# Kernel tuning notes

Hardware: AMD Instinct MI355X
Metric: run time of the kernel (lower is better)

## Reference

```python
import jax, jax.numpy as jnp
import numpy as np

ALPHA, ETA, THETA = 0.999, 0.6, 0.05
EPS = 1e-12  # torch F.normalize eps

def silu(x):
    return x * jax.nn.sigmoid(x)

def l2norm(x):
    # torch.nn.functional.normalize(x) : p=2, dim=1
    n = jnp.linalg.norm(x, axis=1, keepdims=True)
    return x / jnp.maximum(n, EPS)

def mlp(params, x):
    # layers[0]: Linear(16,32)+SiLU ; layers[1]: Linear(32,16)+SiLU
    W0, b0, W1, b1 = params
    h = silu(x @ W0.T + b0)
    return silu(h @ W1.T + b1)

def setup_inputs() -> dict:
    key = jax.random.key(0)
    ks = jax.random.split(key, 8)
    N, D, H = 1048576, 16, 32
    def w(k, shape):
        fan_in = shape[1]
        return jax.random.normal(k, shape, jnp.float32) / np.float32(np.sqrt(fan_in))
    return {
        'X':  jax.random.normal(ks[0], (N, D), jnp.float32),
        'W0': w(ks[1], (H, D)),
        'b0': jnp.zeros((H,), jnp.float32),
        'W1': w(ks[2], (D, H)),
        'b1': jnp.zeros((D,), jnp.float32),
        'WK': w(ks[3], (D, D)),
        'WV': w(ks[4], (D, D)),
        'WQ': w(ks[5], (D, D)),
    }

def reference(X, W0, b0, W1, b1, WK, WV, WQ):
    # ---- update(X): test-time gradient write into the tiny MLP memory ----
    x = jax.lax.stop_gradient(X)            # X.detach()
    v = jax.lax.stop_gradient(silu(x @ WV.T))     # with torch.no_grad()
    q = l2norm(silu(x @ WQ.T))              # normalize(silu(Q(x)))

    def loss_fn(p):
        y = mlp(p, q)
        return jnp.mean((y - v) ** 2)

    g = jax.grad(loss_fn)((W0, b0, W1, b1))
    # surprise starts empty -> zeros; surprise = eta*0 - theta*g = -theta*g
    # update_params = alpha*base.detach() + surprise.detach()
    new_params = tuple(jax.lax.stop_gradient(ALPHA * p - THETA * gi)
                       for p, gi in zip((W0, b0, W1, b1), g))

    # ---- retrieve(X, new_params): key-value read ----
    # note order differs from update: silu(normalize(Q(X)))
    r_in = silu(l2norm(X @ WQ.T))
    return mlp(new_params, r_in)
```

## Files before the change

kernel.cpp:

```cpp
#include <hip/hip_runtime.h>
#include <hip/hip_bf16.h>

typedef __attribute__((ext_vector_type(8))) __bf16 bf16x8;
typedef __attribute__((ext_vector_type(4))) float f32x4;

union U8 { bf16x8 v; unsigned u[4]; uint2 d[2]; };

#define ALPHA 0.999f
#define THETA 0.05f

#define K1_BLOCKS 1536
#define K3_BLOCKS 1536

#define RREC 100
#define F_DY 0
#define F_H  16
#define F_Q  48
#define F_DH 64
#define WAVE_HALFS (32*RREC)
#define K1_SMEM_BYTES 28672

#define R3 100
#define Q_HI 0
#define Q_LO 16
#define H_HI 32
#define H_LO 64

#if __has_builtin(__builtin_amdgcn_rcpf)
#define RCPF(x) __builtin_amdgcn_rcpf(x)
#else
#define RCPF(x) (1.f/(x))
#endif
#if __has_builtin(__builtin_amdgcn_rsqf)
#define RSQF(x) __builtin_amdgcn_rsqf(x)
#else
#define RSQF(x) (1.f/sqrtf(x))
#endif

__device__ __forceinline__ float sigmoidf_(float z){ return RCPF(1.f + __expf(-z)); }

__device__ __forceinline__ unsigned pk2_(float a, float b){
  union { __bf16 h[2]; unsigned u; } x; x.h[0]=(__bf16)a; x.h[1]=(__bf16)b; return x.u;
}
__device__ __forceinline__ float upk_(uint2 p, int r){
  unsigned u = (r<2) ? p.x : p.y;
  return (r&1) ? __uint_as_float(u & 0xffff0000u) : __uint_as_float(u << 16);
}
__device__ __forceinline__ void splitpk_(float a, float b, unsigned &uh, unsigned &ul){
  unsigned h = pk2_(a,b);
  float ah = __uint_as_float(h << 16);
  float bh = __uint_as_float(h & 0xffff0000u);
  uh = h; ul = pk2_(a - ah, b - bh);
}
__device__ __forceinline__ void load_split8_(const float* p, U8 &H, U8 &L){
  const float4 u0 = *(const float4*)p;
  const float4 u1 = *(const float4*)(p+4);
  splitpk_(u0.x,u0.y,H.u[0],L.u[0]); splitpk_(u0.z,u0.w,H.u[1],L.u[1]);
  splitpk_(u1.x,u1.y,H.u[2],L.u[2]); splitpk_(u1.z,u1.w,H.u[3],L.u[3]);
}

__global__ __launch_bounds__(256, 3)
void k1_grad(const float* __restrict__ X,
             const float* __restrict__ W0, const float* __restrict__ b0,
             const float* __restrict__ W1, const float* __restrict__ b1,
             const float* __restrict__ WV, const float* __restrict__ WQ,
             float* __restrict__ wsPart, int N)
{
  __shared__ __align__(16) unsigned char smem_raw[K1_SMEM_BYTES];
  const int tid = threadIdx.x;
  const int w = tid >> 6, l = tid & 63;
  const int g = l >> 4, c = l & 15;
  __bf16* WB = (__bf16*)smem_raw + w*WAVE_HALFS;

  const f32x4 zz = {0.f,0.f,0.f,0.f};

  U8 aWV, aWQ, aW0[2];
  #pragma unroll
  for (int i=0;i<4;++i){ aWV.u[i]=0; aWQ.u[i]=0; aW0[0].u[i]=0; aW0[1].u[i]=0; }
  if (g < 2){
    {
      const float4 u0 = *(const float4*)(WV + c*16 + g*8);
      const float4 u1 = *(const float4*)(WV + c*16 + g*8 + 4);
      aWV.u[0]=pk2_(u0.x,u0.y); aWV.u[1]=pk2_(u0.z,u0.w); aWV.u[2]=pk2_(u1.x,u1.y); aWV.u[3]=pk2_(u1.z,u1.w);
    }
    {
      const float4 u0 = *(const float4*)(WQ + c*16 + g*8);
      const float4 u1 = *(const float4*)(WQ + c*16 + g*8 + 4);
      aWQ.u[0]=pk2_(u0.x,u0.y); aWQ.u[1]=pk2_(u0.z,u0.w); aWQ.u[2]=pk2_(u1.x,u1.y); aWQ.u[3]=pk2_(u1.z,u1.w);
    }
    #pragma unroll
    for (int T=0;T<2;++T){
      const float4 u0 = *(const float4*)(W0 + (16*T + c)*16 + g*8);
      const float4 u1 = *(const float4*)(W0 + (16*T + c)*16 + g*8 + 4);
      aW0[T].u[0]=pk2_(u0.x,u0.y); aW0[T].u[1]=pk2_(u0.z,u0.w); aW0[T].u[2]=pk2_(u1.x,u1.y); aW0[T].u[3]=pk2_(u1.z,u1.w);
    }
  }

  f32x4 acc[4] = {};
  f32x4 bacc1 = {}, bacc0a = {}, bacc0b = {};

  const int nb = N >> 6;
  const int tw = K1_BLOCKS*4;
  const int gw = blockIdx.x*4 + w;
  const int iters = (nb + tw - 1) / tw;

  for (int it = 0; it < iters; ++it) {
    const int batch = gw + it*tw;
    if (batch < nb) {
      const float* xb = X + (size_t)batch*1024;

      #pragma unroll
      for (int hf=0; hf<2; ++hf){
        const float* xh = xb + hf*512;

        #pragma unroll
        for (int t=0;t<2;++t){
          U8 bX;
          if (g < 2){
            const float4 u0 = *(const float4*)(xh + (16*t + c)*16 + g*8);
            const float4 u1 = *(const float4*)(xh + (16*t + c)*16 + g*8 + 4);
            bX.u[0]=pk2_(u0.x,u0.y); bX.u[1]=pk2_(u0.z,u0.w); bX.u[2]=pk2_(u1.x,u1.y); bX.u[3]=pk2_(u1.z,u1.w);
          } else { bX.u[0]=bX.u[1]=bX.u[2]=bX.u[3]=0; }

          f32x4 sv = __builtin_amdgcn_mfma_f32_16x16x32_bf16(aWV.v, bX.v, zz, 0,0,0);
          float v0 = sv[0]*sigmoidf_(sv[0]), v1 = sv[1]*sigmoidf_(sv[1]);
          float v2 = sv[2]*sigmoidf_(sv[2]), v3 = sv[3]*sigmoidf_(sv[3]);
          *(uint2*)(WB + (16*t + c)*RREC + F_DH + 4*g) = make_uint2(pk2_(v0,v1), pk2_(v2,v3));

          f32x4 sq = __builtin_amdgcn_mfma_f32_16x16x32_bf16(aWQ.v, bX.v, zz, 0,0,0);
          f32x4 tq; float n2 = 0.f;
          #pragma unroll
          for (int r=0;r<4;++r){
            float s = sq[r]; float tt = s * sigmoidf_(s);
            tq[r] = tt; n2 = fmaf(tt, tt, n2);
          }
          n2 += __shfl_xor(n2, 16);
          n2 += __shfl_xor(n2, 32);
          const float inv = RSQF(fmaxf(n2, 1e-24f));
          *(uint2*)(WB + (16*t + c)*RREC + F_Q + 4*g) =
              make_uint2(pk2_(tq[0]*inv, tq[1]*inv), pk2_(tq[2]*inv, tq[3]*inv));
        }

        uint2 dshp[2][2];
        {
          const f32x4 b0q0 = *(const f32x4*)(b0 + 4*g);
          const f32x4 b0q1 = *(const f32x4*)(b0 + 16 + 4*g);
          #pragma unroll
          for (int t=0;t<2;++t){
            U8 bq;
            if (g < 2){
              const __bf16* p = WB + (16*t + c)*RREC + F_Q + 8*g;
              bq.d[0] = *(const uint2*)p; bq.d[1] = *(const uint2*)(p + 4);
            } else { bq.u[0]=bq.u[1]=bq.u[2]=bq.u[3]=0; }
            #pragma unroll
            for (int T=0;T<2;++T){
              f32x4 sh = __builtin_amdgcn_mfma_f32_16x16x32_bf16(aW0[T].v, bq.v, T? b0q1 : b0q0, 0,0,0);
              float hh[4], dd[4];
              #pragma unroll
              for (int r=0;r<4;++r){
                float s = sh[r]; float sg = sigmoidf_(s);
                hh[r] = s*sg;
                dd[r] = sg * fmaf(s, 1.f - sg, 1.f);
              }
              *(uint2*)(WB + (16*t + c)*RREC + F_H + 16*T + 4*g) =
                  make_uint2(pk2_(hh[0],hh[1]), pk2_(hh[2],hh[3]));
              dshp[T][t] = make_uint2(pk2_(dd[0],dd[1]), pk2_(dd[2],dd[3]));
            }
          }
        }

        {
          U8 aW1y;
          const float4 u0 = *(const float4*)(W1 + c*32 + g*8);
          const float4 u1 = *(const float4*)(W1 + c*32 + g*8 + 4);
          aW1y.u[0]=pk2_(u0.x,u0.y); aW1y.u[1]=pk2_(u0.z,u0.w); aW1y.u[2]=pk2_(u1.x,u1.y); aW1y.u[3]=pk2_(u1.z,u1.w);
          const f32x4 b1q = *(const f32x4*)(b1 + 4*g);
          #pragma unroll
          for (int t=0;t<2;++t){
            U8 bh;
            const __bf16* p = WB + (16*t + c)*RREC + F_H + 8*g;
            bh.d[0] = *(const uint2*)p; bh.d[1] = *(const uint2*)(p + 4);
            f32x4 sy = __builtin_amdgcn_mfma_f32_16x16x32_bf16(aW1y.v, bh.v, b1q, 0,0,0);
            const uint2 vv = *(const uint2*)(WB + (16*t + c)*RREC + F_DH + 4*g);
            float dyv[4];
            #pragma unroll
            for (int r=0;r<4;++r){
              float s = sy[r]; float sg = sigmoidf_(s);
              float y = s*sg;
              float ds = sg * fmaf(s, 1.f - sg, 1.f);
              dyv[r] = (y - upk_(vv, r)) * ds;
              bacc1[r] += dyv[r];
            }
            *(uint2*)(WB + (16*t + c)*RREC + F_DY + 4*g) =
                make_uint2(pk2_(dyv[0],dyv[1]), pk2_(dyv[2],dyv[3]));
          }
        }

        #pragma unroll
        for (int T=0;T<2;++T){
          U8 aT;
          if (g < 2){
            float t0 = W1[(8*g+0)*32 + 16*T + c], t1 = W1[(8*g+1)*32 + 16*T + c];
            float t2 = W1[(8*g+2)*32 + 16*T + c], t3 = W1[(8*g+3)*32 + 16*T + c];
            float t4 = W1[(8*g+4)*32 + 16*T + c], t5 = W1[(8*g+5)*32 + 16*T + c];
            float t6 = W1[(8*g+6)*32 + 16*T + c], t7 = W1[(8*g+7)*32 + 16*T + c];
            aT.u[0]=pk2_(t0,t1); aT.u[1]=pk2_(t2,t3); aT.u[2]=pk2_(t4,t5); aT.u[3]=pk2_(t6,t7);
          } else { aT.u[0]=aT.u[1]=aT.u[2]=aT.u[3]=0; }
          #pragma unroll
          for (int t=0;t<2;++t){
            U8 bdy;
            if (g < 2){
              const __bf16* p = WB + (16*t + c)*RREC + F_DY + 8*g;
              bdy.d[0] = *(const uint2*)p; bdy.d[1] = *(const uint2*)(p + 4);
            } else { bdy.u[0]=bdy.u[1]=bdy.u[2]=bdy.u[3]=0; }
            f32x4 sd = __builtin_amdgcn_mfma_f32_16x16x32_bf16(aT.v, bdy.v, zz, 0,0,0);
            float d0 = sd[0]*upk_(dshp[T][t],0), d1 = sd[1]*upk_(dshp[T][t],1);
            float d2 = sd[2]*upk_(dshp[T][t],2), d3 = sd[3]*upk_(dshp[T][t],3);
            if (T == 0){ bacc0a[0]+=d0; bacc0a[1]+=d1; bacc0a[2]+=d2; bacc0a[3]+=d3; }
            else       { bacc0b[0]+=d0; bacc0b[1]+=d1; bacc0b[2]+=d2; bacc0b[3]+=d3; }
            *(uint2*)(WB + (16*t + c)*RREC + F_DH + 16*T + 4*g) =
                make_uint2(pk2_(d0,d1), pk2_(d2,d3));
          }
        }

        {
          const __bf16* base = WB + (g*8)*RREC + c;
          {
            bf16x8 fdy, fh0, fh1;
            #pragma unroll
            for (int i=0;i<8;++i){
              const __bf16* pr = base + i*RREC;
              fdy[i] = pr[F_DY];
              fh0[i] = pr[F_H];
              fh1[i] = pr[F_H + 16];
            }
            acc[0] = __builtin_amdgcn_mfma_f32_16x16x32_bf16(fdy, fh0, acc[0], 0,0,0);
            acc[1] = __builtin_amdgcn_mfma_f32_16x16x32_bf16(fdy, fh1, acc[1], 0,0,0);
          }
          {
            bf16x8 fd0, fd1, fq;
            #pragma unroll
            for (int i=0;i<8;++i){
              const __bf16* pr = base + i*RREC;
              fd0[i] = pr[F_DH];
              fd1[i] = pr[F_DH + 16];
              fq[i]  = pr[F_Q];
            }
            acc[2] = __builtin_amdgcn_mfma_f32_16x16x32_bf16(fd0, fq, acc[2], 0,0,0);
            acc[3] = __builtin_amdgcn_mfma_f32_16x16x32_bf16(fd1, fq, acc[3], 0,0,0);
          }
        }
      }
    }
  }

  __syncthreads();
  float* red = (float*)smem_raw;
  #pragma unroll
  for (int r=0;r<4;++r){
    red[w*1792 + 0*256 + l*4 + r] = acc[0][r];
    red[w*1792 + 1*256 + l*4 + r] = acc[1][r];
    red[w*1792 + 2*256 + l*4 + r] = bacc1[r];
    red[w*1792 + 3*256 + l*4 + r] = acc[2][r];
    red[w*1792 + 4*256 + l*4 + r] = acc[3][r];
    red[w*1792 + 5*256 + l*4 + r] = bacc0a[r];
    red[w*1792 + 6*256 + l*4 + r] = bacc0b[r];
  }
  __syncthreads();
  for (int s = tid; s < 1792; s += 256){
    float sum = red[s] + red[1792+s] + red[2*1792+s] + red[3*1792+s];
    wsPart[(size_t)blockIdx.x*1792 + s] = sum;
  }
}

__global__ void k2a_reduce(const float* __restrict__ wsPart, float* __restrict__ tmp)
{
  const int s = blockIdx.x*256 + threadIdx.x;
  const int c = blockIdx.y;
  float g = 0.f;
  #pragma unroll 8
  for (int j=0;j<96;++j) g += wsPart[(size_t)(c*96+j)*1792 + s];
  tmp[(size_t)c*1792 + s] = g;
}

__global__ void k2b_reduce(const float* __restrict__ tmp,
                           const float* __restrict__ W0, const float* __restrict__ b0,
                           const float* __restrict__ W1, const float* __restrict__ b1,
                           float* __restrict__ P, float scale)
{
  int s = blockIdx.x*256 + threadIdx.x;
  if (s >= 1792) return;
  int a = s >> 8, l = (s >> 2) & 63, r = s & 3;
  int m = ((l>>4)<<2) + r, n = l & 15;
  const bool bias = (a==2)||(a==5)||(a==6);
  float g = 0.f;
  if (!bias){
    #pragma unroll
    for (int c=0;c<16;++c) g += tmp[(size_t)c*1792 + s];
  } else if (n == 0){
    const int base = a*256 + ((l>>4)<<6) + r;
    for (int c=0;c<16;++c){
      const float* tc = tmp + (size_t)c*1792 + base;
      #pragma unroll
      for (int nn=0;nn<16;++nn) g += tc[nn*4];
    }
  }
  g *= scale;
  if (a==0)      P[544 + m*32 + n]       = ALPHA*W1[m*32+n]        - THETA*g;
  else if (a==1) P[544 + m*32 + 16 + n]  = ALPHA*W1[m*32+16+n]     - THETA*g;
  else if (a==2){ if (n==0) P[1056 + m]  = ALPHA*b1[m]             - THETA*g; }
  else if (a==3) P[m*16 + n]             = ALPHA*W0[m*16+n]        - THETA*g;
  else if (a==4) P[(16+m)*16 + n]        = ALPHA*W0[(16+m)*16+n]   - THETA*g;
  else if (a==5){ if (n==0) P[512 + m]   = ALPHA*b0[m]             - THETA*g; }
  else           { if (n==0) P[512+16+m] = ALPHA*b0[16+m]          - THETA*g; }
}

__global__ __launch_bounds__(256, 3)
void k3_retrieve(const float* __restrict__ X, const float* __restrict__ WQ,
                 const float* __restrict__ P, float* __restrict__ out, int N)
{
  __shared__ __align__(16) __bf16 smem[4*64*R3];
  const int tid = threadIdx.x;
  const int w = tid >> 6, l = tid & 63;
  const int g = l >> 4, c = l & 15;
  __bf16* WB = smem + w*64*R3;
  const f32x4 zz = {0.f,0.f,0.f,0.f};

  U8 aQh, aQl, aW0h[2], aW0l[2], aW1h, aW1l;
  #pragma unroll
  for (int i=0;i<4;++i){
    aQh.u[i]=aQl.u[i]=0;
    aW0h[0].u[i]=aW0l[0].u[i]=0; aW0h[1].u[i]=aW0l[1].u[i]=0;
  }
  if (g < 2){
    load_split8_(WQ + c*16 + g*8, aQh, aQl);
    #pragma unroll
    for (int T=0;T<2;++T) load_split8_(P + (16*T + c)*16 + g*8, aW0h[T], aW0l[T]);
  }
  load_split8_(P + 544 + c*32 + g*8, aW1h, aW1l);
  const f32x4 b0q0 = *(const f32x4*)(P + 512 + 4*g);
  const f32x4 b0q1 = *(const f32x4*)(P + 528 + 4*g);
  const f32x4 b1q  = *(const f32x4*)(P + 1056 + 4*g);

  const int nb = N >> 6;
  const int tw = K3_BLOCKS*4;
  const int gw = blockIdx.x*4 + w;
  const int iters = (nb + tw - 1) / tw;

  for (int it=0; it<iters; ++it){
    const int batch = gw + it*tw;
    if (batch < nb){
      const float* xb = X + (size_t)batch*1024;

      #pragma unroll
      for (int t=0;t<4;++t){
        U8 bXh, bXl;
        if (g < 2){ load_split8_(xb + (16*t + c)*16 + g*8, bXh, bXl); }
        else { bXh.u[0]=bXh.u[1]=bXh.u[2]=bXh.u[3]=0; bXl=bXh; }
        f32x4 s = __builtin_amdgcn_mfma_f32_16x16x32_bf16(aQl.v, bXh.v, zz, 0,0,0);
        s = __builtin_amdgcn_mfma_f32_16x16x32_bf16(aQh.v, bXl.v, s, 0,0,0);
        s = __builtin_amdgcn_mfma_f32_16x16x32_bf16(aQh.v, bXh.v, s, 0,0,0);
        float n2 = 0.f;
        #pragma unroll
        for (int r=0;r<4;++r) n2 = fmaf(s[r], s[r], n2);
        n2 += __shfl_xor(n2, 16);
        n2 += __shfl_xor(n2, 32);
        const float inv = RSQF(fmaxf(n2, 1e-24f));
        float qv[4];
        #pragma unroll
        for (int r=0;r<4;++r){ float z = s[r]*inv; qv[r] = z * sigmoidf_(z); }
        unsigned qh0,ql0,qh1,ql1;
        splitpk_(qv[0],qv[1],qh0,ql0); splitpk_(qv[2],qv[3],qh1,ql1);
        __bf16* R = WB + (16*t + c)*R3;
        *(uint2*)(R + Q_HI + 4*g) = make_uint2(qh0,qh1);
        *(uint2*)(R + Q_LO + 4*g) = make_uint2(ql0,ql1);
      }

      #pragma unroll
      for (int t=0;t<4;++t){
        U8 bqh, bql;
        if (g < 2){
          const __bf16* p = WB + (16*t + c)*R3;
          bqh.d[0] = *(const uint2*)(p + Q_HI + 8*g); bqh.d[1] = *(const uint2*)(p + Q_HI + 8*g + 4);
          bql.d[0] = *(const uint2*)(p + Q_LO + 8*g); bql.d[1] = *(const uint2*)(p + Q_LO + 8*g + 4);
        } else {
          bqh.u[0]=bqh.u[1]=bqh.u[2]=bqh.u[3]=0; bql=bqh;
        }
        #pragma unroll
        for (int T=0;T<2;++T){
          f32x4 sh = __builtin_amdgcn_mfma_f32_16x16x32_bf16(aW0l[T].v, bqh.v, T? b0q1 : b0q0, 0,0,0);
          sh = __builtin_amdgcn_mfma_f32_16x16x32_bf16(aW0h[T].v, bql.v, sh, 0,0,0);
          sh = __builtin_amdgcn_mfma_f32_16x16x32_bf16(aW0h[T].v, bqh.v, sh, 0,0,0);
          float hv[4];
          #pragma unroll
          for (int r=0;r<4;++r){ float s = sh[r]; hv[r] = s * sigmoidf_(s); }
          unsigned hh0,hl0,hh1,hl1;
          splitpk_(hv[0],hv[1],hh0,hl0); splitpk_(hv[2],hv[3],hh1,hl1);
          __bf16* R = WB + (16*t + c)*R3;
          *(uint2*)(R + H_HI + 16*T + 4*g) = make_uint2(hh0,hh1);
          *(uint2*)(R + H_LO + 16*T + 4*g) = make_uint2(hl0,hl1);
        }
      }

      #pragma unroll
      for (int t=0;t<4;++t){
        U8 bhh, bhl;
        const __bf16* p = WB + (16*t + c)*R3;
        bhh.d[0] = *(const uint2*)(p + H_HI + 8*g); bhh.d[1] = *(const uint2*)(p + H_HI + 8*g + 4);
        bhl.d[0] = *(const uint2*)(p + H_LO + 8*g); bhl.d[1] = *(const uint2*)(p + H_LO + 8*g + 4);
        f32x4 sy = __builtin_amdgcn_mfma_f32_16x16x32_bf16(aW1l.v, bhh.v, b1q, 0,0,0);
        sy = __builtin_amdgcn_mfma_f32_16x16x32_bf16(aW1h.v, bhl.v, sy, 0,0,0);
        sy = __builtin_amdgcn_mfma_f32_16x16x32_bf16(aW1h.v, bhh.v, sy, 0,0,0);
        float4 o;
        o.x = sy[0]*sigmoidf_(sy[0]);
        o.y = sy[1]*sigmoidf_(sy[1]);
        o.z = sy[2]*sigmoidf_(sy[2]);
        o.w = sy[3]*sigmoidf_(sy[3]);
        *(float4*)(out + ((size_t)batch*64 + 16*t + c)*16 + 4*g) = o;
      }
    }
  }
}

extern "C" void kernel_launch(void* const* d_in, const int* in_sizes, int n_in,
                              void* d_out, int out_size, void* d_ws, size_t ws_size,
                              hipStream_t stream)
{
  const float* X  = (const float*)d_in[0];
  const float* W0 = (const float*)d_in[1];
  const float* b0 = (const float*)d_in[2];
  const float* W1 = (const float*)d_in[3];
  const float* b1 = (const float*)d_in[4];
  const float* WV = (const float*)d_in[6];
  const float* WQ = (const float*)d_in[7];
  float* ws   = (float*)d_ws;
  float* P    = ws;
  float* part = ws + 2048;
  float* tmp  = part + (size_t)K1_BLOCKS*1792;

  const int N = in_sizes[0] / 16;
  const float scale = 2.f / (16.f * (float)N);

  k1_grad<<<dim3(K1_BLOCKS), dim3(256), 0, stream>>>(X, W0, b0, W1, b1, WV, WQ, part, N);
  k2a_reduce<<<dim3(7,16), dim3(256), 0, stream>>>(part, tmp);
  k2b_reduce<<<dim3(7), dim3(256), 0, stream>>>(tmp, W0, b0, W1, b1, P, scale);
  k3_retrieve<<<dim3(K3_BLOCKS), dim3(256), 0, stream>>>(X, WQ, P, (float*)d_out, N);
}
```

Measured before the change: 107.4 us.

## Use 32x32x16 MFMA in gradient kernel and compute bias sums via ones-matrix MFMA

Reworks the forward/backward phase of the gradient kernel to use 32x32x16 bf16 MFMAs covering all 32 lanes' rows. This replaces the half-idle 16x16x32 tiles, where lanes with g>=2 fed zeros, and fuses the V and Q projections into one MFMA. Bias gradients are now accumulated by MFMA against a ones vector instead of scalar VALU adds, which lets the second reduction kernel drop its special bias-gathering path. The aim is fewer wasted matrix-core cycles and less VALU work, at the cost of more accumulator registers and a different lane/row mapping.

```diff
diff --git a/kernel.cpp b/kernel.cpp
--- a/kernel.cpp
+++ b/kernel.cpp
@@ -3,6 +3,7 @@
 
 typedef __attribute__((ext_vector_type(8))) __bf16 bf16x8;
 typedef __attribute__((ext_vector_type(4))) float f32x4;
+typedef __attribute__((ext_vector_type(16))) float f32x16;
 
 union U8 { bf16x8 v; unsigned u[4]; uint2 d[2]; };
 
@@ -42,9 +43,8 @@
 __device__ __forceinline__ unsigned pk2_(float a, float b){
   union { __bf16 h[2]; unsigned u; } x; x.h[0]=(__bf16)a; x.h[1]=(__bf16)b; return x.u;
 }
-__device__ __forceinline__ float upk_(uint2 p, int r){
-  unsigned u = (r<2) ? p.x : p.y;
-  return (r&1) ? __uint_as_float(u & 0xffff0000u) : __uint_as_float(u << 16);
+__device__ __forceinline__ float upks_(unsigned u, int s){
+  return s ? __uint_as_float(u & 0xffff0000u) : __uint_as_float(u << 16);
 }
 __device__ __forceinline__ void splitpk_(float a, float b, unsigned &uh, unsigned &ul){
   unsigned h = pk2_(a,b);
@@ -57,6 +57,11 @@
   const float4 u1 = *(const float4*)(p+4);
   splitpk_(u0.x,u0.y,H.u[0],L.u[0]); splitpk_(u0.z,u0.w,H.u[1],L.u[1]);
   splitpk_(u1.x,u1.y,H.u[2],L.u[2]); splitpk_(u1.z,u1.w,H.u[3],L.u[3]);
+}
+__device__ __forceinline__ void pack8f_(const float* p, U8 &A){
+  const float4 u0 = *(const float4*)p;
+  const float4 u1 = *(const float4*)(p+4);
+  A.u[0]=pk2_(u0.x,u0.y); A.u[1]=pk2_(u0.z,u0.w); A.u[2]=pk2_(u1.x,u1.y); A.u[3]=pk2_(u1.z,u1.w);
 }
 
 __global__ __launch_bounds__(256, 3)
@@ -69,35 +74,20 @@
   __shared__ __align__(16) unsigned char smem_raw[K1_SMEM_BYTES];
   const int tid = threadIdx.x;
   const int w = tid >> 6, l = tid & 63;
-  const int g = l >> 4, c = l & 15;
+  const int row = l & 31, hi = l >> 5;
+  const int c16 = l & 15, g16 = l >> 4;
   __bf16* WB = (__bf16*)smem_raw + w*WAVE_HALFS;
 
-  const f32x4 zz = {0.f,0.f,0.f,0.f};
-
-  U8 aWV, aWQ, aW0[2];
+  bf16x8 ones;
   #pragma unroll
-  for (int i=0;i<4;++i){ aWV.u[i]=0; aWQ.u[i]=0; aW0[0].u[i]=0; aW0[1].u[i]=0; }
-  if (g < 2){
-    {
-      const float4 u0 = *(const float4*)(WV + c*16 + g*8);
-      const float4 u1 = *(const float4*)(WV + c*16 + g*8 + 4);
-      aWV.u[0]=pk2_(u0.x,u0.y); aWV.u[1]=pk2_(u0.z,u0.w); aWV.u[2]=pk2_(u1.x,u1.y); aWV.u[3]=pk2_(u1.z,u1.w);
-    }
-    {
-      const float4 u0 = *(const float4*)(WQ + c*16 + g*8);
-      const float4 u1 = *(const float4*)(WQ + c*16 + g*8 + 4);
-      aWQ.u[0]=pk2_(u0.x,u0.y); aWQ.u[1]=pk2_(u0.z,u0.w); aWQ.u[2]=pk2_(u1.x,u1.y); aWQ.u[3]=pk2_(u1.z,u1.w);
-    }
-    #pragma unroll
-    for (int T=0;T<2;++T){
-      const float4 u0 = *(const float4*)(W0 + (16*T + c)*16 + g*8);
-      const float4 u1 = *(const float4*)(W0 + (16*T + c)*16 + g*8 + 4);
-      aW0[T].u[0]=pk2_(u0.x,u0.y); aW0[T].u[1]=pk2_(u0.z,u0.w); aW0[T].u[2]=pk2_(u1.x,u1.y); aW0[T].u[3]=pk2_(u1.z,u1.w);
-    }
-  }
-
-  f32x4 acc[4] = {};
-  f32x4 bacc1 = {}, bacc0a = {}, bacc0b = {};
+  for (int i=0;i<8;++i) ones[i] = (__bf16)1.f;
+
+  U8 aWVQ, aW0p;
+  pack8f_((row < 16) ? (WV + row*16 + hi*8) : (WQ + (row-16)*16 + hi*8), aWVQ);
+  pack8f_(W0 + row*16 + hi*8, aW0p);
+
+  f32x4 accW[4] = {};
+  f32x4 accB1 = {}, accB0a = {}, accB0b = {};
 
   const int nb = N >> 6;
   const int tw = K1_BLOCKS*4;
@@ -112,143 +102,146 @@
       #pragma unroll
       for (int hf=0; hf<2; ++hf){
         const float* xh = xb + hf*512;
-
-        #pragma unroll
-        for (int t=0;t<2;++t){
-          U8 bX;
-          if (g < 2){
-            const float4 u0 = *(const float4*)(xh + (16*t + c)*16 + g*8);
-            const float4 u1 = *(const float4*)(xh + (16*t + c)*16 + g*8 + 4);
-            bX.u[0]=pk2_(u0.x,u0.y); bX.u[1]=pk2_(u0.z,u0.w); bX.u[2]=pk2_(u1.x,u1.y); bX.u[3]=pk2_(u1.z,u1.w);
-          } else { bX.u[0]=bX.u[1]=bX.u[2]=bX.u[3]=0; }
-
-          f32x4 sv = __builtin_amdgcn_mfma_f32_16x16x32_bf16(aWV.v, bX.v, zz, 0,0,0);
-          float v0 = sv[0]*sigmoidf_(sv[0]), v1 = sv[1]*sigmoidf_(sv[1]);
-          float v2 = sv[2]*sigmoidf_(sv[2]), v3 = sv[3]*sigmoidf_(sv[3]);
-          *(uint2*)(WB + (16*t + c)*RREC + F_DH + 4*g) = make_uint2(pk2_(v0,v1), pk2_(v2,v3));
-
-          f32x4 sq = __builtin_amdgcn_mfma_f32_16x16x32_bf16(aWQ.v, bX.v, zz, 0,0,0);
-          f32x4 tq; float n2 = 0.f;
+        __bf16* R = WB + row*RREC;
+
+        U8 bX; pack8f_(xh + row*16 + hi*8, bX);
+        f32x16 c1;
+        #pragma unroll
+        for (int i=0;i<16;++i) c1[i] = 0.f;
+        c1 = __builtin_amdgcn_mfma_f32_32x32x16_bf16(aWVQ.v, bX.v, c1, 0,0,0);
+        unsigned vvp[4];
+        #pragma unroll
+        for (int j=0;j<4;++j){
+          float a = c1[2*j],  sa = a*sigmoidf_(a);
+          float b = c1[2*j+1],sb = b*sigmoidf_(b);
+          vvp[j] = pk2_(sa, sb);
+        }
+        float qv[8]; float n2 = 0.f;
+        #pragma unroll
+        for (int r=0;r<8;++r){
+          float s = c1[8+r]; float t = s*sigmoidf_(s);
+          qv[r] = t; n2 = fmaf(t,t,n2);
+        }
+        n2 += __shfl_xor(n2, 32);
+        const float inv = RSQF(fmaxf(n2, 1e-24f));
+        *(uint2*)(R + F_Q + 4*hi)     = make_uint2(pk2_(qv[0]*inv,qv[1]*inv), pk2_(qv[2]*inv,qv[3]*inv));
+        *(uint2*)(R + F_Q + 8 + 4*hi) = make_uint2(pk2_(qv[4]*inv,qv[5]*inv), pk2_(qv[6]*inv,qv[7]*inv));
+
+        U8 bq;
+        { const __bf16* p = R + F_Q + hi*8;
+          bq.d[0] = *(const uint2*)p; bq.d[1] = *(const uint2*)(p+4); }
+        f32x16 c2;
+        { const float4 bA = *(const float4*)(b0 + 4*hi);
+          const float4 bB = *(const float4*)(b0 + 8 + 4*hi);
+          const float4 bC = *(const float4*)(b0 + 16 + 4*hi);
+          const float4 bD = *(const float4*)(b0 + 24 + 4*hi);
+          c2[0]=bA.x;c2[1]=bA.y;c2[2]=bA.z;c2[3]=bA.w;
+          c2[4]=bB.x;c2[5]=bB.y;c2[6]=bB.z;c2[7]=bB.w;
+          c2[8]=bC.x;c2[9]=bC.y;c2[10]=bC.z;c2[11]=bC.w;
+          c2[12]=bD.x;c2[13]=bD.y;c2[14]=bD.z;c2[15]=bD.w; }
+        c2 = __builtin_amdgcn_mfma_f32_32x32x16_bf16(aW0p.v, bq.v, c2, 0,0,0);
+        unsigned hpk[8], dshp[8];
+        #pragma unroll
+        for (int j=0;j<8;++j){
+          float sa = c2[2*j],   sga = sigmoidf_(sa);
+          float sb = c2[2*j+1], sgb = sigmoidf_(sb);
+          hpk[j]  = pk2_(sa*sga, sb*sgb);
+          dshp[j] = pk2_(sga*fmaf(sa,1.f-sga,1.f), sgb*fmaf(sb,1.f-sgb,1.f));
+        }
+        *(uint2*)(R + F_H + 4*hi)      = make_uint2(hpk[0],hpk[1]);
+        *(uint2*)(R + F_H + 8 + 4*hi)  = make_uint2(hpk[2],hpk[3]);
+        *(uint2*)(R + F_H + 16 + 4*hi) = make_uint2(hpk[4],hpk[5]);
+        *(uint2*)(R + F_H + 24 + 4*hi) = make_uint2(hpk[6],hpk[7]);
+
+        U8 a1, a2;
+        #pragma unroll
+        for (int i=0;i<4;++i){ a1.u[i]=0; a2.u[i]=0; }
+        if (row < 16) pack8f_(W1 + row*32 + hi*8, a1);
+        else          pack8f_(W1 + (row-16)*32 + 16 + hi*8, a2);
+        U8 bhlo, bhhi;
+        { const __bf16* p = R + F_H + hi*8;
+          bhlo.d[0] = *(const uint2*)p; bhlo.d[1] = *(const uint2*)(p+4);
+          const __bf16* p2 = R + F_H + 16 + hi*8;
+          bhhi.d[0] = *(const uint2*)p2; bhhi.d[1] = *(const uint2*)(p2+4); }
+        f32x16 c3;
+        { const float4 bA = *(const float4*)(b1 + 4*hi);
+          const float4 bB = *(const float4*)(b1 + 8 + 4*hi);
+          c3[0]=bA.x;c3[1]=bA.y;c3[2]=bA.z;c3[3]=bA.w;
+          c3[4]=bB.x;c3[5]=bB.y;c3[6]=bB.z;c3[7]=bB.w;
           #pragma unroll
-          for (int r=0;r<4;++r){
-            float s = sq[r]; float tt = s * sigmoidf_(s);
-            tq[r] = tt; n2 = fmaf(tt, tt, n2);
+          for (int i=8;i<16;++i) c3[i]=0.f; }
+        c3 = __builtin_amdgcn_mfma_f32_32x32x16_bf16(a1.v, bhlo.v, c3, 0,0,0);
+        c3 = __builtin_amdgcn_mfma_f32_32x32x16_bf16(a2.v, bhhi.v, c3, 0,0,0);
+        unsigned dypk[4];
+        #pragma unroll
+        for (int j=0;j<4;++j){
+          float d2[2];
+          #pragma unroll
+          for (int e=0;e<2;++e){
+            int r = 2*j+e;
+            float s = c3[r] + c3[r+8];
+            float sg = sigmoidf_(s);
+            float y = s*sg;
+            float ds = sg * fmaf(s, 1.f - sg, 1.f);
+            d2[e] = (y - upks_(vvp[r>>1], r&1)) * ds;
           }
-          n2 += __shfl_xor(n2, 16);
-          n2 += __shfl_xor(n2, 32);
-          const float inv = RSQF(fmaxf(n2, 1e-24f));
-          *(uint2*)(WB + (16*t + c)*RREC + F_Q + 4*g) =
-              make_uint2(pk2_(tq[0]*inv, tq[1]*inv), pk2_(tq[2]*inv, tq[3]*inv));
-        }
-
-        uint2 dshp[2][2];
+          dypk[j] = pk2_(d2[0], d2[1]);
+        }
+        *(uint2*)(R + F_DY + 4*hi)     = make_uint2(dypk[0],dypk[1]);
+        *(uint2*)(R + F_DY + 8 + 4*hi) = make_uint2(dypk[2],dypk[3]);
+
+        U8 aT;
+        { float t0 = W1[(hi*8+0)*32 + row], t1 = W1[(hi*8+1)*32 + row];
+          float t2 = W1[(hi*8+2)*32 + row], t3 = W1[(hi*8+3)*32 + row];
+          float t4 = W1[(hi*8+4)*32 + row], t5 = W1[(hi*8+5)*32 + row];
+          float t6 = W1[(hi*8+6)*32 + row], t7 = W1[(hi*8+7)*32 + row];
+          aT.u[0]=pk2_(t0,t1); aT.u[1]=pk2_(t2,t3); aT.u[2]=pk2_(t4,t5); aT.u[3]=pk2_(t6,t7); }
+        U8 bdy;
+        { const __bf16* p = R + F_DY + hi*8;
+          bdy.d[0] = *(const uint2*)p; bdy.d[1] = *(const uint2*)(p+4); }
+        f32x16 c4;
+        #pragma unroll
+        for (int i=0;i<16;++i) c4[i]=0.f;
+        c4 = __builtin_amdgcn_mfma_f32_32x32x16_bf16(aT.v, bdy.v, c4, 0,0,0);
+        unsigned dhpk[8];
+        #pragma unroll
+        for (int j=0;j<8;++j){
+          float d0 = c4[2*j]   * upks_(dshp[j],0);
+          float d1 = c4[2*j+1] * upks_(dshp[j],1);
+          dhpk[j] = pk2_(d0,d1);
+        }
+        *(uint2*)(R + F_DH + 4*hi)      = make_uint2(dhpk[0],dhpk[1]);
+        *(uint2*)(R + F_DH + 8 + 4*hi)  = make_uint2(dhpk[2],dhpk[3]);
+        *(uint2*)(R + F_DH + 16 + 4*hi) = make_uint2(dhpk[4],dhpk[5]);
+        *(uint2*)(R + F_DH + 24 + 4*hi) = make_uint2(dhpk[6],dhpk[7]);
+
+        const __bf16* gbase = WB + (g16*8)*RREC + c16;
         {
-          const f32x4 b0q0 = *(const f32x4*)(b0 + 4*g);
-          const f32x4 b0q1 = *(const f32x4*)(b0 + 16 + 4*g);
+          bf16x8 fdy, fh0, fh1;
           #pragma unroll
-          for (int t=0;t<2;++t){
-            U8 bq;
-            if (g < 2){
-              const __bf16* p = WB + (16*t + c)*RREC + F_Q + 8*g;
-              bq.d[0] = *(const uint2*)p; bq.d[1] = *(const uint2*)(p + 4);
-            } else { bq.u[0]=bq.u[1]=bq.u[2]=bq.u[3]=0; }
-            #pragma unroll
-            for (int T=0;T<2;++T){
-              f32x4 sh = __builtin_amdgcn_mfma_f32_16x16x32_bf16(aW0[T].v, bq.v, T? b0q1 : b0q0, 0,0,0);
-              float hh[4], dd[4];
-              #pragma unroll
-              for (int r=0;r<4;++r){
-                float s = sh[r]; float sg = sigmoidf_(s);
-                hh[r] = s*sg;
-                dd[r] = sg * fmaf(s, 1.f - sg, 1.f);
-              }
-              *(uint2*)(WB + (16*t + c)*RREC + F_H + 16*T + 4*g) =
-                  make_uint2(pk2_(hh[0],hh[1]), pk2_(hh[2],hh[3]));
-              dshp[T][t] = make_uint2(pk2_(dd[0],dd[1]), pk2_(dd[2],dd[3]));
-            }
+          for (int i=0;i<8;++i){
+            const __bf16* pr = gbase + i*RREC;
+            fdy[i] = pr[F_DY];
+            fh0[i] = pr[F_H];
+            fh1[i] = pr[F_H + 16];
           }
-        }
-
+          accW[0] = __builtin_amdgcn_mfma_f32_16x16x32_bf16(fdy, fh0, accW[0], 0,0,0);
+          accW[1] = __builtin_amdgcn_mfma_f32_16x16x32_bf16(fdy, fh1, accW[1], 0,0,0);
+          accB1   = __builtin_amdgcn_mfma_f32_16x16x32_bf16(fdy, ones, accB1, 0,0,0);
+        }
         {
-          U8 aW1y;
-          const float4 u0 = *(const float4*)(W1 + c*32 + g*8);
-          const float4 u1 = *(const float4*)(W1 + c*32 + g*8 + 4);
-          aW1y.u[0]=pk2_(u0.x,u0.y); aW1y.u[1]=pk2_(u0.z,u0.w); aW1y.u[2]=pk2_(u1.x,u1.y); aW1y.u[3]=pk2_(u1.z,u1.w);
-          const f32x4 b1q = *(const f32x4*)(b1 + 4*g);
+          bf16x8 fd0, fd1, fq;
           #pragma unroll
-          for (int t=0;t<2;++t){
-            U8 bh;
-            const __bf16* p = WB + (16*t + c)*RREC + F_H + 8*g;
-            bh.d[0] = *(const uint2*)p; bh.d[1] = *(const uint2*)(p + 4);
-            f32x4 sy = __builtin_amdgcn_mfma_f32_16x16x32_bf16(aW1y.v, bh.v, b1q, 0,0,0);
-            const uint2 vv = *(const uint2*)(WB + (16*t + c)*RREC + F_DH + 4*g);
-            float dyv[4];
-            #pragma unroll
-            for (int r=0;r<4;++r){
-              float s = sy[r]; float sg = sigmoidf_(s);
-              float y = s*sg;
-              float ds = sg * fmaf(s, 1.f - sg, 1.f);
-              dyv[r] = (y - upk_(vv, r)) * ds;
-              bacc1[r] += dyv[r];
-            }
-            *(uint2*)(WB + (16*t + c)*RREC + F_DY + 4*g) =
-                make_uint2(pk2_(dyv[0],dyv[1]), pk2_(dyv[2],dyv[3]));
+          for (int i=0;i<8;++i){
+            const __bf16* pr = gbase + i*RREC;
+            fd0[i] = pr[F_DH];
+            fd1[i] = pr[F_DH + 16];
+            fq[i]  = pr[F_Q];
           }
-        }
-
-        #pragma unroll
-        for (int T=0;T<2;++T){
-          U8 aT;
-          if (g < 2){
-            float t0 = W1[(8*g+0)*32 + 16*T + c], t1 = W1[(8*g+1)*32 + 16*T + c];
-            float t2 = W1[(8*g+2)*32 + 16*T + c], t3 = W1[(8*g+3)*32 + 16*T + c];
-            float t4 = W1[(8*g+4)*32 + 16*T + c], t5 = W1[(8*g+5)*32 + 16*T + c];
-            float t6 = W1[(8*g+6)*32 + 16*T + c], t7 = W1[(8*g+7)*32 + 16*T + c];
-            aT.u[0]=pk2_(t0,t1); aT.u[1]=pk2_(t2,t3); aT.u[2]=pk2_(t4,t5); aT.u[3]=pk2_(t6,t7);
-          } else { aT.u[0]=aT.u[1]=aT.u[2]=aT.u[3]=0; }
-          #pragma unroll
-          for (int t=0;t<2;++t){
-            U8 bdy;
-            if (g < 2){
-              const __bf16* p = WB + (16*t + c)*RREC + F_DY + 8*g;
-              bdy.d[0] = *(const uint2*)p; bdy.d[1] = *(const uint2*)(p + 4);
-            } else { bdy.u[0]=bdy.u[1]=bdy.u[2]=bdy.u[3]=0; }
-            f32x4 sd = __builtin_amdgcn_mfma_f32_16x16x32_bf16(aT.v, bdy.v, zz, 0,0,0);
-            float d0 = sd[0]*upk_(dshp[T][t],0), d1 = sd[1]*upk_(dshp[T][t],1);
-            float d2 = sd[2]*upk_(dshp[T][t],2), d3 = sd[3]*upk_(dshp[T][t],3);
-            if (T == 0){ bacc0a[0]+=d0; bacc0a[1]+=d1; bacc0a[2]+=d2; bacc0a[3]+=d3; }
-            else       { bacc0b[0]+=d0; bacc0b[1]+=d1; bacc0b[2]+=d2; bacc0b[3]+=d3; }
-            *(uint2*)(WB + (16*t + c)*RREC + F_DH + 16*T + 4*g) =
-                make_uint2(pk2_(d0,d1), pk2_(d2,d3));
-          }
-        }
-
-        {
-          const __bf16* base = WB + (g*8)*RREC + c;
-          {
-            bf16x8 fdy, fh0, fh1;
-            #pragma unroll
-            for (int i=0;i<8;++i){
-              const __bf16* pr = base + i*RREC;
-              fdy[i] = pr[F_DY];
-              fh0[i] = pr[F_H];
-              fh1[i] = pr[F_H + 16];
-            }
-            acc[0] = __builtin_amdgcn_mfma_f32_16x16x32_bf16(fdy, fh0, acc[0], 0,0,0);
-            acc[1] = __builtin_amdgcn_mfma_f32_16x16x32_bf16(fdy, fh1, acc[1], 0,0,0);
-          }
-          {
-            bf16x8 fd0, fd1, fq;
-            #pragma unroll
-            for (int i=0;i<8;++i){
-              const __bf16* pr = base + i*RREC;
-              fd0[i] = pr[F_DH];
-              fd1[i] = pr[F_DH + 16];
-              fq[i]  = pr[F_Q];
-            }
-            acc[2] = __builtin_amdgcn_mfma_f32_16x16x32_bf16(fd0, fq, acc[2], 0,0,0);
-            acc[3] = __builtin_amdgcn_mfma_f32_16x16x32_bf16(fd1, fq, acc[3], 0,0,0);
-          }
+          accW[2] = __builtin_amdgcn_mfma_f32_16x16x32_bf16(fd0, fq, accW[2], 0,0,0);
+          accW[3] = __builtin_amdgcn_mfma_f32_16x16x32_bf16(fd1, fq, accW[3], 0,0,0);
+          accB0a  = __builtin_amdgcn_mfma_f32_16x16x32_bf16(fd0, ones, accB0a, 0,0,0);
+          accB0b  = __builtin_amdgcn_mfma_f32_16x16x32_bf16(fd1, ones, accB0b, 0,0,0);
         }
       }
     }
@@ -258,13 +251,13 @@
   float* red = (float*)smem_raw;
   #pragma unroll
   for (int r=0;r<4;++r){
-    red[w*1792 + 0*256 + l*4 + r] = acc[0][r];
-    red[w*1792 + 1*256 + l*4 + r] = acc[1][r];
-    red[w*1792 + 2*256 + l*4 + r] = bacc1[r];
-    red[w*1792 + 3*256 + l*4 + r] = acc[2][r];
-    red[w*1792 + 4*256 + l*4 + r] = acc[3][r];
-    red[w*1792 + 5*256 + l*4 + r] = bacc0a[r];
-    red[w*1792 + 6*256 + l*4 + r] = bacc0b[r];
+    red[w*1792 + 0*256 + l*4 + r] = accW[0][r];
+    red[w*1792 + 1*256 + l*4 + r] = accW[1][r];
+    red[w*1792 + 2*256 + l*4 + r] = accB1[r];
+    red[w*1792 + 3*256 + l*4 + r] = accW[2][r];
+    red[w*1792 + 4*256 + l*4 + r] = accW[3][r];
+    red[w*1792 + 5*256 + l*4 + r] = accB0a[r];
+    red[w*1792 + 6*256 + l*4 + r] = accB0b[r];
   }
   __syncthreads();
   for (int s = tid; s < 1792; s += 256){
@@ -290,22 +283,12 @@
 {
   int s = blockIdx.x*256 + threadIdx.x;
   if (s >= 1792) return;
+  float g = 0.f;
+  #pragma unroll
+  for (int c=0;c<16;++c) g += tmp[(size_t)c*1792 + s];
+  g *= scale;
   int a = s >> 8, l = (s >> 2) & 63, r = s & 3;
   int m = ((l>>4)<<2) + r, n = l & 15;
-  const bool bias = (a==2)||(a==5)||(a==6);
-  float g = 0.f;
-  if (!bias){
-    #pragma unroll
-    for (int c=0;c<16;++c) g += tmp[(size_t)c*1792 + s];
-  } else if (n == 0){
-    const int base = a*256 + ((l>>4)<<6) + r;
-    for (int c=0;c<16;++c){
-      const float* tc = tmp + (size_t)c*1792 + base;
-      #pragma unroll
-      for (int nn=0;nn<16;++nn) g += tc[nn*4];
-    }
-  }
-  g *= scale;
   if (a==0)      P[544 + m*32 + n]       = ALPHA*W1[m*32+n]        - THETA*g;
   else if (a==1) P[544 + m*32 + 16 + n]  = ALPHA*W1[m*32+16+n]     - THETA*g;
   else if (a==2){ if (n==0) P[1056 + m]  = ALPHA*b1[m]             - THETA*g; }
```

Result: faster. 94.62 us (-11.9%).
